# Kernel tuning notes

Hardware: AMD Instinct MI355X
Metric: run time of the kernel (lower is better)

Reference implementation:

```python
import jax, jax.numpy as jnp
import numpy as np

DIM = 256
HEADS = 8
DIM_HEAD = 32
INNER = HEADS * DIM_HEAD
K_NEIGHBORS = 16
TEMPERATURE = 1.0
SCALE = DIM_HEAD ** (-0.5)
BATCH = 512
N_FEATURES = 32


def setup_inputs() -> dict:
    key = jax.random.key(0)
    ks = jax.random.split(key, 6)
    s = 0.02
    return {
        "x": jax.random.normal(ks[0], (BATCH, N_FEATURES, DIM), dtype=jnp.float32),
        "W_qkv": jax.random.normal(ks[1], (DIM, 3 * INNER), dtype=jnp.float32) * s,
        "W_out": jax.random.normal(ks[2], (INNER, DIM), dtype=jnp.float32) * s,
        "b_out": jnp.zeros((DIM,), dtype=jnp.float32),
        "W_repr": jax.random.normal(ks[3], (DIM, DIM), dtype=jnp.float32) * s,
        "b_repr": jnp.zeros((DIM,), dtype=jnp.float32),
    }


def reference(x, W_qkv, W_out, b_out, W_repr, b_repr):
    B, n, d = x.shape
    # A. sample representations: mean over features + linear proj
    reprs = jnp.mean(x, axis=1) @ W_repr + b_repr  # [B, dim]
    # B. kNN graph via cosine similarity
    normed = reprs / jnp.linalg.norm(reprs, axis=-1, keepdims=True)
    sim_mat = (normed @ normed.T) / TEMPERATURE  # [B, B]
    k_actual = min(K_NEIGHBORS + 1, B)
    _, knn_idx = jax.lax.top_k(sim_mat, k_actual)  # [B, k+1]
    # C. attention mask: 0 for self+neighbors, -inf elsewhere
    neg_inf = jnp.float32(-jnp.inf)
    mask = jnp.full((B, B), neg_inf, dtype=jnp.float32)
    mask = mask.at[jnp.arange(B)[:, None], knn_idx].set(0.0)  # [B, B]
    # D. masked cross-sample attention (vectorized over all features/heads)
    qkv = x @ W_qkv  # [B, n, 3*inner]
    q, k, v = jnp.split(qkv, 3, axis=-1)
    def to_bhnd(t):
        return t.reshape(B, n, HEADS, DIM_HEAD).transpose(0, 2, 1, 3)  # b h n d
    q, k, v = to_bhnd(q), to_bhnd(k), to_bhnd(v)
    # per-feature cross-sample scores: [n, b, h, B]
    sim = jnp.einsum('bhnd,Bhnd->nbhB', q, k) * SCALE
    sim = sim + mask[None, :, None, :]
    attn = jax.nn.softmax(sim, axis=-1)
    out = jnp.einsum('nbhB,Bhnd->bnhd', attn, v)  # [b, n, h, d]
    out = out.reshape(B, n, INNER)
    return out @ W_out + b_out
```

## Files before the change

### kernel.cpp

```cpp
#include <hip/hip_runtime.h>
#include <math.h>

#define DIMX 256
#define NFEAT 32
#define BATCH 512
#define HEADS 8
#define DHEAD 32
#define KNN 17
#define QKV_W 768
#define SCALE_L2 0.25503486f

typedef unsigned int uint;
typedef unsigned short ushort_t;
typedef __attribute__((ext_vector_type(8))) short short8_t;
typedef __attribute__((ext_vector_type(4))) float float4_t;

__device__ inline float bf_lo(uint u) { return __uint_as_float(u << 16); }
__device__ inline float bf_hi(uint u) { return __uint_as_float(u & 0xffff0000u); }
__device__ inline ushort_t f2bf(float f) {
  uint u = __float_as_uint(f);
  return (ushort_t)((u + 0x7fffu + ((u >> 16) & 1u)) >> 16);
}

#if defined(__has_builtin)
#if __has_builtin(__builtin_amdgcn_fdot2_f32_bf16)
#define HAVE_DOT2 1
#endif
#if __has_builtin(__builtin_amdgcn_exp2f)
#define EXP2(x) __builtin_amdgcn_exp2f(x)
#endif
#endif
#ifndef EXP2
#define EXP2(x) exp2f(x)
#endif

#ifdef HAVE_DOT2
typedef __attribute__((ext_vector_type(2))) __bf16 bf16x2_t;
__device__ inline float dot2bf(uint a, uint b, float c) {
  return __builtin_amdgcn_fdot2_f32_bf16(
      __builtin_bit_cast(bf16x2_t, a), __builtin_bit_cast(bf16x2_t, b), c, false);
}
#else
__device__ inline float dot2bf(uint a, uint b, float c) {
  return c + bf_lo(a)*bf_lo(b) + bf_hi(a)*bf_hi(b);
}
#endif

__device__ inline void gload16(const ushort_t* g, ushort_t* l) {
  __builtin_amdgcn_global_load_lds(
      (const __attribute__((address_space(1))) void*)g,
      (__attribute__((address_space(3))) void*)l, 16, 0, 0);
}

__global__ __launch_bounds__(256, 2) void repr_prep_kernel(
    const float* __restrict__ x, const float* __restrict__ W_repr,
    const float* __restrict__ b_repr, const float* __restrict__ Wq,
    const float* __restrict__ Wo, float* __restrict__ normed,
    ushort_t* __restrict__ xbf, ushort_t* __restrict__ wqT, ushort_t* __restrict__ woT) {
  __shared__ float smem[64*65];
  int bid = blockIdx.x, t = threadIdx.x;
  if (bid < BATCH) {
    float* mean_s = smem;
    float* red = smem + 256;
    int b = bid;
    float s = 0.f;
#pragma unroll
    for (int n = 0; n < NFEAT; ++n) {
      float v = x[(size_t)(b*NFEAT+n)*DIMX + t];
      s += v;
      xbf[(size_t)(b*NFEAT+n)*DIMX + t] = f2bf(v);
    }
    mean_s[t] = s * (1.0f/NFEAT);
    __syncthreads();
    float acc = b_repr[t];
    for (int d = 0; d < DIMX; ++d) acc += mean_s[d] * W_repr[d*DIMX + t];
    red[t] = acc*acc;
    __syncthreads();
    for (int off = 128; off > 0; off >>= 1) {
      if (t < off) red[t] += red[t+off];
      __syncthreads();
    }
    normed[b*DIMX + t] = acc / sqrtf(red[0]);
  } else {
    int pb = bid - BATCH;
    const float* W; ushort_t* WT; int NN, tx, ty;
    if (pb < 48) { W = Wq; WT = wqT; NN = QKV_W; tx = pb % 12; ty = pb / 12; }
    else { int b2 = pb - 48; W = Wo; WT = woT; NN = DIMX; tx = b2 % 4; ty = b2 / 4; }
    float (*tile)[65] = (float(*)[65])smem;
#pragma unroll
    for (int i = 0; i < 4; ++i) {
      int c = t + 256*i;
      int r = c >> 4, c4 = (c & 15) * 4;
      *(float4*)&tile[r][c4] = *(const float4*)&W[(size_t)(ty*64 + r)*NN + tx*64 + c4];
    }
    __syncthreads();
    int rr = t >> 2, cc0 = (t & 3) * 16;
    uint ow[8];
#pragma unroll
    for (int k = 0; k < 8; ++k)
      ow[k] = (uint)f2bf(tile[cc0 + 2*k][rr]) | ((uint)f2bf(tile[cc0 + 2*k + 1][rr]) << 16);
    uint4 o0 = {ow[0], ow[1], ow[2], ow[3]};
    uint4 o1 = {ow[4], ow[5], ow[6], ow[7]};
    size_t obase = (size_t)(tx*64 + rr)*DIMX + ty*64 + cc0;
    *(uint4*)&WT[obase]     = o0;
    *(uint4*)&WT[obase + 8] = o1;
  }
}

template<bool OUTF32>
__device__ __forceinline__ void gemm_body(
    ushort_t (&As)[2][128][64], ushort_t (&Bs)[2][128][64],
    const ushort_t* __restrict__ A, const ushort_t* __restrict__ Bt,
    void* __restrict__ Cout, const float* __restrict__ bias,
    int M, int N, int K, int row0, int col0) {
  int t = threadIdx.x, l = t & 63, w = t >> 6;
  int wr = w >> 1, wc = w & 1;
  int srcRow = l >> 3, srcCol = (l & 7) * 8;
  float4_t acc[4][4] = {};
  int nkt = K >> 6;
#pragma unroll
  for (int i = 0; i < 4; ++i) {
    int ar = w*32 + i*8;
    gload16(&A [(size_t)(row0+ar+srcRow)*K + srcCol], &As[0][ar][0]);
    gload16(&Bt[(size_t)(col0+ar+srcRow)*K + srcCol], &Bs[0][ar][0]);
  }
  __syncthreads();
  int cur = 0;
  for (int kt = 0; kt < nkt; ++kt) {
    if (kt + 1 < nkt) {
      int k1 = (kt + 1) << 6;
#pragma unroll
      for (int i = 0; i < 4; ++i) {
        int ar = w*32 + i*8;
        gload16(&A [(size_t)(row0+ar+srcRow)*K + k1 + srcCol], &As[cur^1][ar][0]);
        gload16(&Bt[(size_t)(col0+ar+srcRow)*K + k1 + srcCol], &Bs[cur^1][ar][0]);
      }
    }
#pragma unroll
    for (int ks = 0; ks < 2; ++ks) {
      int kk = ks*32 + (l >> 4)*8;
      short8_t a[4], b[4];
#pragma unroll
      for (int m = 0; m < 4; ++m) a[m] = *(short8_t*)&As[cur][wr*64 + m*16 + (l & 15)][kk];
#pragma unroll
      for (int n = 0; n < 4; ++n) b[n] = *(short8_t*)&Bs[cur][wc*64 + n*16 + (l & 15)][kk];
#pragma unroll
      for (int m = 0; m < 4; ++m)
#pragma unroll
        for (int n = 0; n < 4; ++n)
          acc[m][n] = __builtin_amdgcn_mfma_f32_16x16x32_bf16(a[m], b[n], acc[m][n], 0, 0, 0);
    }
    __syncthreads();
    cur ^= 1;
  }
  int crow = (l >> 4) * 4, ccol = l & 15;
#pragma unroll
  for (int m = 0; m < 4; ++m)
#pragma unroll
    for (int n = 0; n < 4; ++n) {
      int col = col0 + wc*64 + n*16 + ccol;
#pragma unroll
      for (int r = 0; r < 4; ++r) {
        int row = row0 + wr*64 + m*16 + crow + r;
        if (OUTF32) ((float*)Cout)[(size_t)row*N + col] = acc[m][n][r] + bias[col];
        else        ((ushort_t*)Cout)[(size_t)row*N + col] = f2bf(acc[m][n][r]);
      }
    }
}

template<bool OUTF32>
__global__ __launch_bounds__(256, 2) void mfma_gemm(
    const ushort_t* __restrict__ A, const ushort_t* __restrict__ Bt,
    void* __restrict__ Cout, const float* __restrict__ bias, int M, int N, int K) {
  __shared__ ushort_t As[2][128][64];
  __shared__ ushort_t Bs[2][128][64];
  gemm_body<OUTF32>(As, Bs, A, Bt, Cout, bias, M, N, K, blockIdx.x*128, blockIdx.y*128);
}

__global__ __launch_bounds__(256, 2) void simqkv_kernel(
    const ushort_t* __restrict__ xbf, const ushort_t* __restrict__ wqT,
    ushort_t* __restrict__ qkv, const float* __restrict__ normed,
    float* __restrict__ sims) {
  __shared__ ushort_t As[2][128][64];
  __shared__ ushort_t Bs[2][128][64];
  int bid = blockIdx.x, t = threadIdx.x;
  if (bid < 768) {
    gemm_body<false>(As, Bs, xbf, wqT, qkv, nullptr, 16384, QKV_W, DIMX,
                     (bid & 127) * 128, (bid >> 7) * 128);
  } else {
    int sid = bid - 768;
    int i0 = (sid & 15) * 32, j0 = (sid >> 4) * 32;
    float (*sA)[68] = (float(*)[68])(&As[0][0][0]);
    float (*sB)[68] = (float(*)[68])(&Bs[0][0][0]);
    int tx = t & 15, ty = t >> 4;
    float acc00 = 0.f, acc01 = 0.f, acc10 = 0.f, acc11 = 0.f;
    for (int k0 = 0; k0 < DIMX; k0 += 64) {
#pragma unroll
      for (int c = t; c < 512; c += 256) {
        int r = c >> 4, cc = (c & 15) * 4;
        *(float4*)&sA[r][cc] = *(const float4*)&normed[(size_t)(i0 + r)*DIMX + k0 + cc];
        *(float4*)&sB[r][cc] = *(const float4*)&normed[(size_t)(j0 + r)*DIMX + k0 + cc];
      }
      __syncthreads();
#pragma unroll 16
      for (int kk = 0; kk < 64; ++kk) {
        float a0 = sA[ty*2][kk],   a1 = sA[ty*2+1][kk];
        float b0 = sB[tx*2][kk],   b1 = sB[tx*2+1][kk];
        acc00 += a0*b0; acc01 += a0*b1; acc10 += a1*b0; acc11 += a1*b1;
      }
      __syncthreads();
    }
    sims[(size_t)(i0+ty*2  )*BATCH + j0+tx*2  ] = acc00;
    sims[(size_t)(i0+ty*2  )*BATCH + j0+tx*2+1] = acc01;
    sims[(size_t)(i0+ty*2+1)*BATCH + j0+tx*2  ] = acc10;
    sims[(size_t)(i0+ty*2+1)*BATCH + j0+tx*2+1] = acc11;
  }
}

__global__ __launch_bounds__(256, 8) void topk_rank(const float* __restrict__ sims,
                                                    int* __restrict__ knn) {
  int i = blockIdx.x, t = threadIdx.x;
  __shared__ float row[BATCH];
  row[t]       = sims[(size_t)i*BATCH + t];
  row[t + 256] = sims[(size_t)i*BATCH + t + 256];
  __syncthreads();
  float v1 = row[t], v2 = row[t + 256];
  int i1 = t, i2 = t + 256;
  int r1 = 0, r2 = 0;
  const float4* r4 = (const float4*)row;
#pragma unroll 8
  for (int c = 0; c < BATCH/4; ++c) {
    float4 q = r4[c];
    int base = c * 4;
    r1 += (q.x > v1 || (q.x == v1 && base+0 < i1));
    r1 += (q.y > v1 || (q.y == v1 && base+1 < i1));
    r1 += (q.z > v1 || (q.z == v1 && base+2 < i1));
    r1 += (q.w > v1 || (q.w == v1 && base+3 < i1));
    r2 += (q.x > v2 || (q.x == v2 && base+0 < i2));
    r2 += (q.y > v2 || (q.y == v2 && base+1 < i2));
    r2 += (q.z > v2 || (q.z == v2 && base+2 < i2));
    r2 += (q.w > v2 || (q.w == v2 && base+3 < i2));
  }
  if (r1 < KNN) knn[i*32 + r1] = i1;
  if (r2 < KNN) knn[i*32 + r2] = i2;
}

#define NF_BLK 8
__global__ __launch_bounds__(256, 8) void attn_kernel(
    const ushort_t* __restrict__ qkv, const int* __restrict__ knn,
    ushort_t* __restrict__ attn_out) {
  int b = blockIdx.x, g = blockIdx.y, t = threadIdx.x;
  int n0 = g * NF_BLK;
  __shared__ float sc_s[2][KNN][HEADS];
  __shared__ int idxp[KNN];
  if (t < KNN) idxp[t] = knn[b*32 + t] * (NFEAT*QKV_W);
  __syncthreads();

  for (int np = 0; np < NF_BLK; np += 2) {
    int n = n0 + np;
    for (int job = t; job < 2*KNN*HEADS; job += 256) {
      int f = (job >= KNN*HEADS) ? 1 : 0;
      int r = job - f*KNN*HEADS;
      int j = r >> 3, h = r & 7;
      const uint4* qp = (const uint4*)&qkv[(size_t)(b*NFEAT + n + f)*QKV_W + h*DHEAD];
      const uint4* kp = (const uint4*)&qkv[(size_t)(idxp[j] + (n + f)*QKV_W + 256 + h*DHEAD)];
      float s0 = 0.f, s1 = 0.f;
#pragma unroll
      for (int i = 0; i < 4; ++i) {
        uint4 qv = qp[i], kv = kp[i];
        s0 = dot2bf(kv.x, qv.x, s0); s1 = dot2bf(kv.y, qv.y, s1);
        s0 = dot2bf(kv.z, qv.z, s0); s1 = dot2bf(kv.w, qv.w, s1);
      }
      sc_s[f][j][h] = (s0 + s1) * SCALE_L2;
    }
    __syncthreads();
    {
      int f = t >> 7, p = t & 127, h = p >> 4;
      float sv[KNN];
#pragma unroll
      for (int j = 0; j < KNN; ++j) sv[j] = sc_s[f][j][h];
      float m = sv[0];
#pragma unroll
      for (int j = 1; j < KNN; ++j) m = fmaxf(m, sv[j]);
      float sum = 0.f;
#pragma unroll
      for (int j = 0; j < KNN; ++j) { sv[j] = EXP2(sv[j] - m); sum += sv[j]; }
      float inv = 1.0f / sum;
      int voff = (n + f)*QKV_W + 512 + p*2;
      float alo = 0.f, ahi = 0.f;
#pragma unroll
      for (int j = 0; j < KNN; ++j) {
        uint wv = *(const uint*)&qkv[(size_t)(idxp[j] + voff)];
        alo += sv[j] * bf_lo(wv);
        ahi += sv[j] * bf_hi(wv);
      }
      *(uint*)&attn_out[(size_t)(b*NFEAT + n + f)*DIMX + p*2] =
          (uint)f2bf(alo * inv) | ((uint)f2bf(ahi * inv) << 16);
    }
    __syncthreads();
  }
}

extern "C" void kernel_launch(void* const* d_in, const int* in_sizes, int n_in,
                              void* d_out, int out_size, void* d_ws, size_t ws_size,
                              hipStream_t stream) {
  const float* x      = (const float*)d_in[0];
  const float* W_qkv  = (const float*)d_in[1];
  const float* W_out  = (const float*)d_in[2];
  const float* b_out  = (const float*)d_in[3];
  const float* W_repr = (const float*)d_in[4];
  const float* b_repr = (const float*)d_in[5];
  float* out = (float*)d_out;

  ushort_t* qkv      = (ushort_t*)d_ws;
  ushort_t* xbf      = qkv + (size_t)16384*QKV_W;
  ushort_t* wqT      = xbf + (size_t)16384*DIMX;
  ushort_t* woT      = wqT + (size_t)QKV_W*DIMX;
  ushort_t* attn_out = woT + (size_t)DIMX*DIMX;
  float*    normed   = (float*)(attn_out + (size_t)16384*DIMX);
  float*    sims     = normed + (size_t)BATCH*DIMX;
  int*      knn      = (int*)(sims + (size_t)BATCH*BATCH);

  repr_prep_kernel<<<BATCH + 64, 256, 0, stream>>>(
      x, W_repr, b_repr, W_qkv, W_out, normed, xbf, wqT, woT);
  simqkv_kernel<<<768 + 256, 256, 0, stream>>>(xbf, wqT, qkv, normed, sims);
  topk_rank<<<BATCH, 256, 0, stream>>>(sims, knn);
  attn_kernel<<<dim3(BATCH, NFEAT/NF_BLK), 256, 0, stream>>>(qkv, knn, attn_out);
  mfma_gemm<true><<<dim3(128, 2), 256, 0, stream>>>(
      attn_out, woT, out, b_out, 16384, DIMX, DIMX);
}
```

Before: 94.28 us.

## Fuse top-k ranking into attention kernel and remap GEMM block order

Removes the separate topk_rank launch by having each attention block recompute the kNN ranking of its similarity row directly into shared memory. The top-k work is now done four times per sample, once per feature group. The attention grid is linearized and swizzled so that feature groups of nearby samples run together. The QKV and output GEMMs now walk N fastest across block IDs, so blocks sharing an A row tile are adjacent, which should improve L2 reuse of A. This trades redundant rank computation for one fewer kernel launch and no knn round trip through global memory.

After: 127.3 us. 35.0% more time.

```diff
diff --git a/kernel.cpp b/kernel.cpp
--- a/kernel.cpp
+++ b/kernel.cpp
@@ -174,7 +174,7 @@
     void* __restrict__ Cout, const float* __restrict__ bias, int M, int N, int K) {
   __shared__ ushort_t As[2][128][64];
   __shared__ ushort_t Bs[2][128][64];
-  gemm_body<OUTF32>(As, Bs, A, Bt, Cout, bias, M, N, K, blockIdx.x*128, blockIdx.y*128);
+  gemm_body<OUTF32>(As, Bs, A, Bt, Cout, bias, M, N, K, blockIdx.y*128, blockIdx.x*128);
 }
 
 __global__ __launch_bounds__(256, 2) void simqkv_kernel(
@@ -186,7 +186,7 @@
   int bid = blockIdx.x, t = threadIdx.x;
   if (bid < 768) {
     gemm_body<false>(As, Bs, xbf, wqT, qkv, nullptr, 16384, QKV_W, DIMX,
-                     (bid & 127) * 128, (bid >> 7) * 128);
+                     (bid / 6) * 128, (bid % 6) * 128);
   } else {
     int sid = bid - 768;
     int i0 = (sid & 15) * 32, j0 = (sid >> 4) * 32;
@@ -217,43 +217,42 @@
   }
 }
 
-__global__ __launch_bounds__(256, 8) void topk_rank(const float* __restrict__ sims,
-                                                    int* __restrict__ knn) {
-  int i = blockIdx.x, t = threadIdx.x;
-  __shared__ float row[BATCH];
-  row[t]       = sims[(size_t)i*BATCH + t];
-  row[t + 256] = sims[(size_t)i*BATCH + t + 256];
-  __syncthreads();
-  float v1 = row[t], v2 = row[t + 256];
-  int i1 = t, i2 = t + 256;
-  int r1 = 0, r2 = 0;
-  const float4* r4 = (const float4*)row;
-#pragma unroll 8
-  for (int c = 0; c < BATCH/4; ++c) {
-    float4 q = r4[c];
-    int base = c * 4;
-    r1 += (q.x > v1 || (q.x == v1 && base+0 < i1));
-    r1 += (q.y > v1 || (q.y == v1 && base+1 < i1));
-    r1 += (q.z > v1 || (q.z == v1 && base+2 < i1));
-    r1 += (q.w > v1 || (q.w == v1 && base+3 < i1));
-    r2 += (q.x > v2 || (q.x == v2 && base+0 < i2));
-    r2 += (q.y > v2 || (q.y == v2 && base+1 < i2));
-    r2 += (q.z > v2 || (q.z == v2 && base+2 < i2));
-    r2 += (q.w > v2 || (q.w == v2 && base+3 < i2));
-  }
-  if (r1 < KNN) knn[i*32 + r1] = i1;
-  if (r2 < KNN) knn[i*32 + r2] = i2;
-}
-
 #define NF_BLK 8
 __global__ __launch_bounds__(256, 8) void attn_kernel(
-    const ushort_t* __restrict__ qkv, const int* __restrict__ knn,
+    const ushort_t* __restrict__ qkv, const float* __restrict__ sims,
     ushort_t* __restrict__ attn_out) {
-  int b = blockIdx.x, g = blockIdx.y, t = threadIdx.x;
+  int bid = blockIdx.x, t = threadIdx.x;
+  int xg = bid & 7, rq = bid >> 3;
+  int g = rq & 3, mq = rq >> 2;
+  int b = xg + (mq << 3);
   int n0 = g * NF_BLK;
   __shared__ float sc_s[2][KNN][HEADS];
   __shared__ int idxp[KNN];
-  if (t < KNN) idxp[t] = knn[b*32 + t] * (NFEAT*QKV_W);
+  __shared__ float srow[BATCH];
+  srow[t]       = sims[(size_t)b*BATCH + t];
+  srow[t + 256] = sims[(size_t)b*BATCH + t + 256];
+  __syncthreads();
+  {
+    float v1 = srow[t], v2 = srow[t + 256];
+    int i1 = t, i2 = t + 256;
+    int r1 = 0, r2 = 0;
+    const float4* r4 = (const float4*)srow;
+#pragma unroll 8
+    for (int c = 0; c < BATCH/4; ++c) {
+      float4 q = r4[c];
+      int base = c * 4;
+      r1 += (q.x > v1 || (q.x == v1 && base+0 < i1));
+      r1 += (q.y > v1 || (q.y == v1 && base+1 < i1));
+      r1 += (q.z > v1 || (q.z == v1 && base+2 < i1));
+      r1 += (q.w > v1 || (q.w == v1 && base+3 < i1));
+      r2 += (q.x > v2 || (q.x == v2 && base+0 < i2));
+      r2 += (q.y > v2 || (q.y == v2 && base+1 < i2));
+      r2 += (q.z > v2 || (q.z == v2 && base+2 < i2));
+      r2 += (q.w > v2 || (q.w == v2 && base+3 < i2));
+    }
+    if (r1 < KNN) idxp[r1] = i1 * (NFEAT*QKV_W);
+    if (r2 < KNN) idxp[r2] = i2 * (NFEAT*QKV_W);
+  }
   __syncthreads();
 
   for (int np = 0; np < NF_BLK; np += 2) {
@@ -319,13 +318,11 @@
   ushort_t* attn_out = woT + (size_t)DIMX*DIMX;
   float*    normed   = (float*)(attn_out + (size_t)16384*DIMX);
   float*    sims     = normed + (size_t)BATCH*DIMX;
-  int*      knn      = (int*)(sims + (size_t)BATCH*BATCH);
 
   repr_prep_kernel<<<BATCH + 64, 256, 0, stream>>>(
       x, W_repr, b_repr, W_qkv, W_out, normed, xbf, wqT, woT);
   simqkv_kernel<<<768 + 256, 256, 0, stream>>>(xbf, wqT, qkv, normed, sims);
-  topk_rank<<<BATCH, 256, 0, stream>>>(sims, knn);
-  attn_kernel<<<dim3(BATCH, NFEAT/NF_BLK), 256, 0, stream>>>(qkv, knn, attn_out);
-  mfma_gemm<true><<<dim3(128, 2), 256, 0, stream>>>(
+  attn_kernel<<<2048, 256, 0, stream>>>(qkv, sims, attn_out);
+  mfma_gemm<true><<<dim3(2, 128), 256, 0, stream>>>(
       attn_out, woT, out, b_out, 16384, DIMX, DIMX);
 }
```
